# Optimization experiments

Hardware: AMD Instinct MI355X
Metric: run time of the kernel (lower is better)

## Reference

```python
import jax, jax.numpy as jnp
import numpy as np

Q = 4096  # num_quantizing
E = 256   # quantizing_dim


def setup_inputs() -> dict:
    key = jax.random.key(0)
    kx, kw = jax.random.split(key)
    x = jax.random.normal(kx, (16, 2048, E), dtype=jnp.float32)
    # nn.init.normal_(weight, mean=0.0, std=0.001)
    weight = 0.001 * jax.random.normal(kw, (Q, E), dtype=jnp.float32)
    return {"x": x, "weight": weight}


def reference(x, weight):
    # x: (*, E), weight: (Q, E)
    input_shape = x.shape
    xf = x.reshape(-1, weight.shape[1])  # (N, E)
    # Squared L2 distance via norm expansion (same argmin as sum(delta^2)):
    x2 = jnp.sum(xf * xf, axis=1, keepdims=True)          # (N, 1)
    w2 = jnp.sum(weight * weight, axis=1)                  # (Q,)
    dist = x2 - 2.0 * (xf @ weight.T) + w2                 # (N, Q)
    q_idx = jnp.argmin(dist, axis=1)                       # (N,)
    q_data = weight[q_idx]                                 # (N, E)
    return q_data.reshape(input_shape), q_idx.reshape(input_shape[:-1])
```

## Files before the change

### kernel.cpp

```cpp
#include <hip/hip_runtime.h>
#include <cfloat>
#include <climits>

constexpr int E  = 256;
constexpr int Qn = 4096;
constexpr float WSCALE = 4096.0f;


typedef _Float16 half8  __attribute__((ext_vector_type(8)));
typedef _Float16 half4v __attribute__((ext_vector_type(4)));
typedef float    f32x16 __attribute__((ext_vector_type(16)));

#define GAS __attribute__((address_space(1)))
#define LAS __attribute__((address_space(3)))

#define NEG_INF __int_as_float(0xFF800000)

__device__ inline bool lexlt(float a, int ai, float b, int bi) {
    return a < b || (a == b && ai < bi);
}

__global__ __launch_bounds__(256) void prep_kernel(
    const float* __restrict__ x, const float* __restrict__ w,
    _Float16* __restrict__ A16, _Float16* __restrict__ B16,
    float* __restrict__ w2, int nxblocks)
{
    int blk  = blockIdx.x;
    int sub  = threadIdx.x >> 6;
    int lane = threadIdx.x & 63;
    bool isX = blk < nxblocks;
    int row  = (isX ? blk : blk - nxblocks) * 4 + sub;

    const float* src = isX ? x : w;
    float4 v = *(const float4*)(src + (size_t)row * E + lane * 4);

    if (!isX) {
        float s = v.x * v.x + v.y * v.y + v.z * v.z + v.w * v.w;
        #pragma unroll
        for (int off = 32; off; off >>= 1) s += __shfl_xor(s, off);
        if (lane == 0) w2[row] = s;
    }

    float sc = isX ? 1.0f : WSCALE;
    half4v h = { (_Float16)(v.x * sc), (_Float16)(v.y * sc),
                 (_Float16)(v.z * sc), (_Float16)(v.w * sc) };
    _Float16* dst16 = (isX ? A16 : B16) + (size_t)row * 256;
    *(half4v*)(dst16 + lane * 4) = h;
}

__device__ inline void ins4max(float K[4], float k) {
    #pragma unroll
    for (int t = 0; t < 4; ++t) {
        float mx = fmaxf(K[t], k);
        k = fminf(K[t], k);
        K[t] = mx;
    }
}

union SmemU {
    struct { _Float16 W[256 * 64]; _Float16 X[256 * 64]; } st[2];
    float2 mergeS[256 * 2 * 4];
};

__global__ __launch_bounds__(512, 2) void vq_mfma_kernel(
    const _Float16* __restrict__ A16,
    const _Float16* __restrict__ B16,
    float4* __restrict__ top4)
{
    __shared__ SmemU sm;

    const int tid  = threadIdx.x;
    const int w    = tid >> 6;
    const int lane = tid & 63;
    const int l31  = lane & 31;
    const int lh   = lane >> 5;
    const int cwg  = blockIdx.x;
    const int rb   = blockIdx.y;

    const int wm = w & 1;
    const int wn = w >> 1;

    f32x16 acc[4][2];
    #pragma unroll
    for (int m = 0; m < 4; ++m)
        #pragma unroll
        for (int n = 0; n < 2; ++n)
            #pragma unroll
            for (int r = 0; r < 16; ++r) acc[m][n][r] = 0.0f;

    const _Float16* Ab16 = A16 + (size_t)rb  * 256 * 256;
    const _Float16* Bb16 = B16 + (size_t)cwg * 256 * 256;

    const int srow = lane >> 3;
    const int schk = lane & 7;

    auto stage = [&](int kt, int b) {
        #pragma unroll
        for (int inst = 0; inst < 4; ++inst) {
            int drow = w * 32 + inst * 8 + srow;
            int gchk = schk ^ (drow & 7);
            const _Float16* gW = Bb16 + (size_t)drow * 256 + kt * 64 + gchk * 8;
            const _Float16* gX = Ab16 + (size_t)drow * 256 + kt * 64 + gchk * 8;
            __builtin_amdgcn_global_load_lds((const GAS void*)gW,
                (LAS void*)(sm.st[b].W + w * 2048 + inst * 512), 16, 0, 0);
            __builtin_amdgcn_global_load_lds((const GAS void*)gX,
                (LAS void*)(sm.st[b].X + w * 2048 + inst * 512), 16, 0, 0);
        }
    };

    stage(0, 0);
    __syncthreads();

    #pragma unroll
    for (int kt = 0; kt < 4; ++kt) {
        const int b = kt & 1;
        if (kt < 3) stage(kt + 1, b ^ 1);

        const _Float16* Wb = sm.st[b].W;
        const _Float16* Xb = sm.st[b].X;

        __builtin_amdgcn_s_setprio(1);
        #pragma unroll
        for (int s = 0; s < 4; ++s) {
            const int kc = 2 * s + lh;
            half8 wf[4], xf[2];
            #pragma unroll
            for (int m = 0; m < 4; ++m) {
                int fr = wm * 128 + m * 32 + l31;
                wf[m] = *(const half8*)(Wb + fr * 64 + ((kc ^ (fr & 7)) << 3));
            }
            #pragma unroll
            for (int n = 0; n < 2; ++n) {
                int xr = wn * 64 + n * 32 + l31;
                xf[n] = *(const half8*)(Xb + xr * 64 + ((kc ^ (xr & 7)) << 3));
            }
            #pragma unroll
            for (int m = 0; m < 4; ++m)
                #pragma unroll
                for (int n = 0; n < 2; ++n)
                    acc[m][n] = __builtin_amdgcn_mfma_f32_32x32x16_f16(
                        wf[m], xf[n], acc[m][n], 0, 0, 0);
        }
        __builtin_amdgcn_s_setprio(0);
        __syncthreads();
    }

    float t1[2][2], t2[2][2];
    #pragma unroll
    for (int g2 = 0; g2 < 2; ++g2)
        #pragma unroll
        for (int n = 0; n < 2; ++n) { t1[g2][n] = NEG_INF; t2[g2][n] = NEG_INF; }

    #pragma unroll
    for (int m = 0; m < 4; ++m) {
        const int g2 = m >> 1;
        #pragma unroll
        for (int r = 0; r < 16; ++r) {
            int crow = (r & 3) + 8 * (r >> 2) + 4 * lh;
            int qg   = cwg * 256 + wm * 128 + m * 32 + crow;
            #pragma unroll
            for (int n = 0; n < 2; ++n) {
                float pk = __int_as_float(
                    (__float_as_int(acc[m][n][r]) & 0xFFFFF000) | qg);
                t2[g2][n] = __builtin_amdgcn_fmed3f(t1[g2][n], t2[g2][n], pk);
                t1[g2][n] = fmaxf(t1[g2][n], pk);
            }
        }
    }

    #pragma unroll
    for (int n = 0; n < 2; ++n) {
        int xrow = wn * 64 + n * 32 + l31;
        #pragma unroll
        for (int g2 = 0; g2 < 2; ++g2)
            sm.mergeS[(xrow * 2 + wm) * 4 + (lh * 2 + g2)] =
                make_float2(t1[g2][n], t2[g2][n]);
    }
    __syncthreads();

    {
        int xrow = tid >> 1, cgl = tid & 1;
        float K[4] = { NEG_INF, NEG_INF, NEG_INF, NEG_INF };
        #pragma unroll
        for (int sl = 0; sl < 4; ++sl) {
            float2 a = sm.mergeS[(xrow * 2 + cgl) * 4 + sl];
            ins4max(K, a.x);
            ins4max(K, a.y);
        }
        top4[(size_t)(rb * 256 + xrow) * 32 + cwg * 2 + cgl] =
            make_float4(K[0], K[1], K[2], K[3]);
    }
}

__global__ __launch_bounds__(256) void finalize_kernel(
    const float4* __restrict__ top4, const float* __restrict__ x,
    const float* __restrict__ w, const float* __restrict__ w2,
    float* __restrict__ qdata, float* __restrict__ qidx)
{
    int row  = blockIdx.x * 4 + (threadIdx.x >> 6);
    int lane = threadIdx.x & 63;

    float cand[4];
    if (lane < 32) {
        float4 c4 = top4[(size_t)row * 32 + lane];
        cand[0] = c4.x; cand[1] = c4.y; cand[2] = c4.z; cand[3] = c4.w;
    } else {
        cand[0] = cand[1] = cand[2] = cand[3] = NEG_INF;
    }

    int chosen[4];
    #pragma unroll
    for (int p = 0; p < 4; ++p) {
        float cur = fmaxf(fmaxf(cand[0], cand[1]), fmaxf(cand[2], cand[3]));
        #pragma unroll
        for (int off = 32; off; off >>= 1)
            cur = fmaxf(cur, __shfl_xor(cur, off));
        int curb = __float_as_int(cur);
        chosen[p] = curb & 0xFFF;
        #pragma unroll
        for (int j = 0; j < 4; ++j)
            if (__float_as_int(cand[j]) == curb) cand[j] = NEG_INF;
    }

    float4 xv = *(const float4*)(x + (size_t)row * E + lane * 4);
    float s2 = xv.x * xv.x + xv.y * xv.y + xv.z * xv.z + xv.w * xv.w;
    float d[4];
    #pragma unroll
    for (int j = 0; j < 4; ++j) {
        float4 wv = *(const float4*)(w + (size_t)chosen[j] * E + lane * 4);
        d[j] = xv.x * wv.x + xv.y * wv.y + xv.z * wv.z + xv.w * wv.w;
    }
    #pragma unroll
    for (int off = 32; off; off >>= 1) {
        s2 += __shfl_xor(s2, off);
        #pragma unroll
        for (int j = 0; j < 4; ++j) d[j] += __shfl_xor(d[j], off);
    }

    float bs = FLT_MAX; int win = INT_MAX;
    #pragma unroll
    for (int j = 0; j < 4; ++j) {
        float s = (s2 - 2.0f * d[j]) + w2[chosen[j]];
        if (lexlt(s, chosen[j], bs, win)) { bs = s; win = chosen[j]; }
    }

    if (lane == 0) qidx[row] = (float)win;
    *(float4*)(qdata + (size_t)row * E + lane * 4) =
        *(const float4*)(w + (size_t)win * E + lane * 4);
}

constexpr int FBM = 64, FBN = 128, FBK = 64, FPAD = 4, FTH = 256;

__global__ __launch_bounds__(64) void row_sumsq_kernel(const float* __restrict__ src,
                                                       float* __restrict__ dst) {
    int row = blockIdx.x, lane = threadIdx.x;
    float4 v = ((const float4*)(src + (size_t)row * E))[lane];
    float s = v.x * v.x + v.y * v.y + v.z * v.z + v.w * v.w;
    #pragma unroll
    for (int off = 32; off > 0; off >>= 1) s += __shfl_down(s, off);
    if (lane == 0) dst[row] = s;
}

__global__ __launch_bounds__(FTH) void vq_fallback_kernel(
    const float* __restrict__ x, const float* __restrict__ w,
    const float* __restrict__ x2, const float* __restrict__ w2,
    float* __restrict__ qdata, float* __restrict__ qidx)
{
    __shared__ float xs[FBM][FBK + FPAD];
    __shared__ float ws[FBN][FBK + FPAD];
    __shared__ float redS[FBM][16];
    __shared__ int   redC[FBM][16];
    __shared__ int   bestC[FBM];

    const int tid = threadIdx.x, tr = tid >> 4, tc = tid & 15;
    const int r0 = blockIdx.x * FBM;
    float best[4]; int bidx[4];
    #pragma unroll
    for (int i = 0; i < 4; ++i) { best[i] = FLT_MAX; bidx[i] = 0x7FFFFFFF; }
    float x2r[4];
    #pragma unroll
    for (int i = 0; i < 4; ++i) x2r[i] = x2[r0 + tr + 16 * i];

    for (int qt = 0; qt < Qn / FBN; ++qt) {
        const int c0 = qt * FBN;
        float acc[4][8];
        #pragma unroll
        for (int i = 0; i < 4; ++i)
            #pragma unroll
            for (int j = 0; j < 8; ++j) acc[i][j] = 0.f;
        for (int kt = 0; kt < E / FBK; ++kt) {
            __syncthreads();
            const int kk = (tid & 15) * 4, rr = tid >> 4;
            #pragma unroll
            for (int m = 0; m < 4; ++m)
                *(float4*)&xs[m * 16 + rr][kk] =
                    *(const float4*)(x + (size_t)(r0 + m * 16 + rr) * E + kt * FBK + kk);
            #pragma unroll
            for (int m = 0; m < 8; ++m)
                *(float4*)&ws[m * 16 + rr][kk] =
                    *(const float4*)(w + (size_t)(c0 + m * 16 + rr) * E + kt * FBK + kk);
            __syncthreads();
            #pragma unroll
            for (int k4 = 0; k4 < FBK / 4; ++k4) {
                float4 a[4], bb[8];
                #pragma unroll
                for (int i = 0; i < 4; ++i) a[i] = *(const float4*)&xs[tr + 16 * i][k4 * 4];
                #pragma unroll
                for (int j = 0; j < 8; ++j) bb[j] = *(const float4*)&ws[tc + 16 * j][k4 * 4];
                #pragma unroll
                for (int i = 0; i < 4; ++i)
                    #pragma unroll
                    for (int j = 0; j < 8; ++j) {
                        acc[i][j] += a[i].x * bb[j].x; acc[i][j] += a[i].y * bb[j].y;
                        acc[i][j] += a[i].z * bb[j].z; acc[i][j] += a[i].w * bb[j].w;
                    }
            }
        }
        #pragma unroll
        for (int i = 0; i < 4; ++i)
            #pragma unroll
            for (int j = 0; j < 8; ++j) {
                int c = c0 + tc + 16 * j;
                float s = (x2r[i] - 2.0f * acc[i][j]) + w2[c];
                if (s < best[i]) { best[i] = s; bidx[i] = c; }
            }
    }
    #pragma unroll
    for (int i = 0; i < 4; ++i) { redS[tr + 16 * i][tc] = best[i]; redC[tr + 16 * i][tc] = bidx[i]; }
    __syncthreads();
    if (tid < FBM) {
        float bs = FLT_MAX; int bc = 0x7FFFFFFF;
        #pragma unroll
        for (int t = 0; t < 16; ++t) {
            float s = redS[tid][t]; int c = redC[tid][t];
            if (s < bs || (s == bs && c < bc)) { bs = s; bc = c; }
        }
        qidx[r0 + tid] = (float)bc; bestC[tid] = bc;
    }
    __syncthreads();
    for (int it = 0; it < FBM / 4; ++it) {
        int row = it * 4 + (tid >> 6), c = bestC[row], kk = (tid & 63) * 4;
        *(float4*)(qdata + (size_t)(r0 + row) * E + kk) = *(const float4*)(w + (size_t)c * E + kk);
    }
}

extern "C" void kernel_launch(void* const* d_in, const int* in_sizes, int n_in,
                              void* d_out, int out_size, void* d_ws, size_t ws_size,
                              hipStream_t stream) {
    const float* x = (const float*)d_in[0];
    const float* w = (const float*)d_in[1];
    const int N = in_sizes[0] / E;

    float* qdata = (float*)d_out;
    float* qidx  = (float*)d_out + (size_t)N * E;

    size_t off = 0;
    auto carve = [&](size_t bytes) { size_t p = off; off += (bytes + 255) & ~(size_t)255; return p; };
    size_t oA16 = carve((size_t)N  * 256 * sizeof(_Float16));
    size_t oB16 = carve((size_t)Qn * 256 * sizeof(_Float16));
    size_t ow2  = carve((size_t)Qn * sizeof(float));
    size_t oT   = carve((size_t)N * 32 * sizeof(float4));
    size_t ox2f = carve((size_t)N * sizeof(float));

    if (ws_size >= off && (N % 256) == 0) {
        char* ws = (char*)d_ws;
        _Float16* A16 = (_Float16*)(ws + oA16);
        _Float16* B16 = (_Float16*)(ws + oB16);
        float* w2    = (float*)(ws + ow2);
        float4* top4 = (float4*)(ws + oT);

        prep_kernel<<<N / 4 + Qn / 4, 256, 0, stream>>>(x, w, A16, B16, w2, N / 4);
        vq_mfma_kernel<<<dim3(Qn / 256, N / 256), 512, 0, stream>>>(A16, B16, top4);
        finalize_kernel<<<N / 4, 256, 0, stream>>>(top4, x, w, w2, qdata, qidx);
    } else {
        float* x2 = (float*)d_ws;
        float* w2 = x2 + N;
        row_sumsq_kernel<<<N, 64, 0, stream>>>(x, x2);
        row_sumsq_kernel<<<Qn, 64, 0, stream>>>(w, w2);
        vq_fallback_kernel<<<N / FBM, FTH, 0, stream>>>(x, w, x2, w2, qdata, qidx);
    }
}
```

Baseline: 199.7 us.

## Restructure K-loop into 4-slot half-tile pipeline with fine-grained vmcnt waits

Splits each 64-wide K tile into two 32-wide halves held in a 4-slot LDS ring, prefetching three stages ahead. Replaces __syncthreads with raw s_barrier plus explicit vmcnt/lgkmcnt waits so global-to-LDS loads overlap more MFMA work. The LDS swizzle is rearranged for the 32-wide rows. The aim is to hide load latency that the double-buffered loop exposed, at the cost of more barriers per tile and fragile hand-counted waits.

```diff
diff --git a/kernel.cpp b/kernel.cpp
--- a/kernel.cpp
+++ b/kernel.cpp
@@ -58,7 +58,7 @@
 }
 
 union SmemU {
-    struct { _Float16 W[256 * 64]; _Float16 X[256 * 64]; } st[2];
+    struct { _Float16 W[8192]; _Float16 X[8192]; } slot[4];
     float2 mergeS[256 * 2 * 4];
 };
 
@@ -91,58 +91,69 @@
     const _Float16* Ab16 = A16 + (size_t)rb  * 256 * 256;
     const _Float16* Bb16 = B16 + (size_t)cwg * 256 * 256;
 
-    const int srow = lane >> 3;
-    const int schk = lane & 7;
-
-    auto stage = [&](int kt, int b) {
-        #pragma unroll
-        for (int inst = 0; inst < 4; ++inst) {
-            int drow = w * 32 + inst * 8 + srow;
-            int gchk = schk ^ (drow & 7);
-            const _Float16* gW = Bb16 + (size_t)drow * 256 + kt * 64 + gchk * 8;
-            const _Float16* gX = Ab16 + (size_t)drow * 256 + kt * 64 + gchk * 8;
-            __builtin_amdgcn_global_load_lds((const GAS void*)gW,
-                (LAS void*)(sm.st[b].W + w * 2048 + inst * 512), 16, 0, 0);
-            __builtin_amdgcn_global_load_lds((const GAS void*)gX,
-                (LAS void*)(sm.st[b].X + w * 2048 + inst * 512), 16, 0, 0);
-        }
+    const int sdrow = lane >> 2;
+    const int schk  = lane & 3;
+    auto stage = [&](int hj, int i) {
+        int slot = hj & 3, kt = hj >> 1, h = hj & 1;
+        int drow = i * 128 + w * 16 + sdrow;
+        int gchk = schk ^ ((drow >> 1) & 3);
+        size_t koff = (size_t)kt * 64 + h * 32 + gchk * 8;
+        const _Float16* gW = Bb16 + (size_t)drow * 256 + koff;
+        const _Float16* gX = Ab16 + (size_t)drow * 256 + koff;
+        _Float16* dW = sm.slot[slot].W + i * 4096 + w * 512;
+        _Float16* dX = sm.slot[slot].X + i * 4096 + w * 512;
+        __builtin_amdgcn_global_load_lds((const GAS void*)gW, (LAS void*)dW, 16, 0, 0);
+        __builtin_amdgcn_global_load_lds((const GAS void*)gX, (LAS void*)dX, 16, 0, 0);
     };
 
-    stage(0, 0);
-    __syncthreads();
-
-    #pragma unroll
-    for (int kt = 0; kt < 4; ++kt) {
-        const int b = kt & 1;
-        if (kt < 3) stage(kt + 1, b ^ 1);
-
-        const _Float16* Wb = sm.st[b].W;
-        const _Float16* Xb = sm.st[b].X;
+    stage(0, 0); stage(0, 1);
+    stage(1, 0); stage(1, 1);
+    stage(2, 0); stage(2, 1);
+    asm volatile("s_waitcnt vmcnt(8)" ::: "memory");
+    __builtin_amdgcn_s_barrier();
+
+    #pragma unroll
+    for (int p = 0; p < 16; ++p) {
+        const int hj  = p >> 1;
+        const int q   = p & 1;
+        const int slot = hj & 3;
+        const int kcl = 2 * q + lh;
+
+        half8 wf[4], xf[2];
+        #pragma unroll
+        for (int m = 0; m < 4; ++m) {
+            int fr = wm * 128 + m * 32 + l31;
+            wf[m] = *(const half8*)(sm.slot[slot].W
+                        + fr * 32 + ((kcl ^ ((fr >> 1) & 3)) << 3));
+        }
+        #pragma unroll
+        for (int n = 0; n < 2; ++n) {
+            int xr = wn * 64 + n * 32 + l31;
+            xf[n] = *(const half8*)(sm.slot[slot].X
+                        + xr * 32 + ((kcl ^ ((xr >> 1) & 3)) << 3));
+        }
+
+        if (hj + 3 <= 7) stage(hj + 3, q);
+
+        __builtin_amdgcn_s_barrier();
+        asm volatile("s_waitcnt lgkmcnt(0)" ::: "memory");
+        __builtin_amdgcn_sched_barrier(0);
 
         __builtin_amdgcn_s_setprio(1);
         #pragma unroll
-        for (int s = 0; s < 4; ++s) {
-            const int kc = 2 * s + lh;
-            half8 wf[4], xf[2];
-            #pragma unroll
-            for (int m = 0; m < 4; ++m) {
-                int fr = wm * 128 + m * 32 + l31;
-                wf[m] = *(const half8*)(Wb + fr * 64 + ((kc ^ (fr & 7)) << 3));
-            }
-            #pragma unroll
-            for (int n = 0; n < 2; ++n) {
-                int xr = wn * 64 + n * 32 + l31;
-                xf[n] = *(const half8*)(Xb + xr * 64 + ((kc ^ (xr & 7)) << 3));
-            }
-            #pragma unroll
-            for (int m = 0; m < 4; ++m)
-                #pragma unroll
-                for (int n = 0; n < 2; ++n)
-                    acc[m][n] = __builtin_amdgcn_mfma_f32_32x32x16_f16(
-                        wf[m], xf[n], acc[m][n], 0, 0, 0);
-        }
+        for (int m = 0; m < 4; ++m)
+            #pragma unroll
+            for (int n = 0; n < 2; ++n)
+                acc[m][n] = __builtin_amdgcn_mfma_f32_32x32x16_f16(
+                    wf[m], xf[n], acc[m][n], 0, 0, 0);
         __builtin_amdgcn_s_setprio(0);
-        __syncthreads();
+
+        if (q == 1) {
+            if (hj <= 4)      asm volatile("s_waitcnt vmcnt(8)" ::: "memory");
+            else if (hj == 5) asm volatile("s_waitcnt vmcnt(4)" ::: "memory");
+            else if (hj == 6) asm volatile("s_waitcnt vmcnt(0)" ::: "memory");
+        }
+        __builtin_amdgcn_s_barrier();
     }
 
     float t1[2][2], t2[2][2];
```

New measurement: 209.6 us. 5.0% more time.
